# Kernel tuning notes

Measured on AMD Instinct MI355X. Metric: run time of the kernel, lower is better.

Reference implementation:

```python
import jax, jax.numpy as jnp
import numpy as np

H, D, L = 4, 64, 7          # heads, hidden, seq_len (SEQ_LEN+2)
B = 32768                    # batch
VOCAB = 6
NOUT = 2 * 5 + 1             # 2*SEQ_LEN+1 = 11
EPS = 1e-5


def _ln(x, g, b):
    m = jnp.mean(x, axis=-1, keepdims=True)
    v = jnp.var(x, axis=-1, keepdims=True)
    return (x - m) / jnp.sqrt(v + EPS) * g + b


def _mha(q, k, v, wq, wk, wv, wo, bo):
    # wq/wk/wv: [H, D, D]; q: [B, Lq, D]; k,v: [B, Lk, D]
    qh = jnp.einsum('bqd,hde->hbqe', q, wq)
    kh = jnp.einsum('bkd,hde->hbke', k, wk)
    vh = jnp.einsum('bkd,hde->hbke', v, wv)
    s = jnp.einsum('hbqe,hbke->hbqk', qh, kh) / jnp.sqrt(jnp.asarray(D, q.dtype))
    # NOTE: original torch code softmaxes over dim=1 of [B,Lq,Lk] = the QUERY axis
    a = jax.nn.softmax(s, axis=2)
    o = jnp.einsum('hbqk,hbke->hbqe', a, vh)
    o = jnp.transpose(o, (1, 2, 0, 3)).reshape(q.shape[0], q.shape[1], H * D)
    return o @ wo + bo


def setup_inputs() -> dict:
    key = jax.random.key(0)
    ks = iter(jax.random.split(key, 32))
    n = lambda shape, s=0.02: jax.random.normal(next(ks), shape, dtype=jnp.float32) * s
    inp = {
        'tokens': jax.random.randint(next(ks), (B, L), 0, VOCAB, dtype=jnp.int32),
        'emb': n((VOCAB, D), 1.0),
        'pos': n((L, 1), 1.0),
        'qparam': n((1, D), 1.0),
        'in_w': n((D + 1, D)), 'in_b': n((D,)),
        # encoding layer (num_encoding_layers=1)
        'e_wq': n((H, D, D)), 'e_wk': n((H, D, D)), 'e_wv': n((H, D, D)),
        'e_wo': n((H * D, D)), 'e_bo': n((D,)),
        'e_g1': jnp.ones((D,), jnp.float32), 'e_b1': jnp.zeros((D,), jnp.float32),
        'e_c1w': n((D, 2 * D)), 'e_c1b': n((2 * D,)),
        'e_c2w': n((2 * D, D)), 'e_c2b': n((D,)),
        'e_g2': jnp.ones((D,), jnp.float32), 'e_b2': jnp.zeros((D,), jnp.float32),
        # decoder MHA
        'd_wq': n((H, D, D)), 'd_wk': n((H, D, D)), 'd_wv': n((H, D, D)),
        'd_wo': n((H * D, D)), 'd_bo': n((D,)),
        'fc_w': n((D, NOUT)), 'fc_b': n((NOUT,)),
    }
    return inp


def reference(tokens, emb, pos, qparam, in_w, in_b,
              e_wq, e_wk, e_wv, e_wo, e_bo, e_g1, e_b1,
              e_c1w, e_c1b, e_c2w, e_c2b, e_g2, e_b2,
              d_wq, d_wk, d_wv, d_wo, d_bo, fc_w, fc_b):
    x = emb[tokens]                                   # [B, L, D]
    p = jnp.broadcast_to(pos[None], (x.shape[0], L, 1))
    x = jnp.concatenate([x, p], axis=-1)              # [B, L, D+1]
    x = x @ in_w + in_b                               # Conv1d k=1 == linear
    # encoding layer
    x = _mha(x, x, x, e_wq, e_wk, e_wv, e_wo, e_bo)
    x = _ln(x, e_g1, e_b1)
    x1 = jax.nn.relu(x @ e_c1w + e_c1b)
    x1 = jax.nn.relu(x1 @ e_c2w + e_c2b)
    x = _ln(x + x1, e_g2, e_b2)
    # decoder: single learned query
    q = jnp.broadcast_to(qparam[None], (x.shape[0], 1, D))
    x = _mha(q, x, x, d_wq, d_wk, d_wv, d_wo, d_bo)   # [B, 1, D]
    x = x[:, 0, :]
    return x @ fc_w + fc_b                            # [B, 11]
```

## Files before the change

### kernel.cpp

```cpp
#include <hip/hip_runtime.h>
#include <hip/hip_bf16.h>

#define DEV __device__ __forceinline__

typedef __attribute__((ext_vector_type(8)))  short bf8v;
typedef __attribute__((ext_vector_type(16))) float f16v;
typedef __attribute__((ext_vector_type(4)))  float f4v;

static constexpr int NOUT = 11;

DEV unsigned short b16(float f){
  __hip_bfloat16 h = __float2bfloat16(f);
  unsigned short s; __builtin_memcpy(&s, &h, 2); return s;
}
DEV float bf2f(unsigned short s){
  __hip_bfloat16 h; __builtin_memcpy(&h, &s, 2); return __bfloat162float(h);
}
template<bool BF16>
DEV float ldw(const void* p, int i){
  if constexpr (BF16) return bf2f(((const unsigned short*)p)[i]);
  else return ((const float*)p)[i];
}
DEV f16v MF(bf8v a, bf8v b, f16v c){
  return __builtin_amdgcn_mfma_f32_32x32x16_bf16(a, b, c, 0, 0, 0);
}
DEV f16v zf(){ f16v v; 
  #pragma unroll
  for (int i=0;i<16;++i) v[i] = 0.f; 
  return v; }


__global__ void k_flag(const void* g1, unsigned* flag){
  if (threadIdx.x == 0){
    unsigned bits = *(const unsigned*)g1;
    *flag = (bits == 0x3F800000u) ? 0u : 1u;
  }
}

struct RawW {
  const void *in_w, *in_b, *pos;
  const void *e_wq, *e_wk, *e_wv, *e_wo, *e_bo;
  const void *g1, *b1, *c1w, *c1b, *c2w, *c2b, *g2, *b2;
};
struct PackP {
  unsigned short *Wt, *Mt, *Ut, *C1t, *C2t;
  float *BB;
};

template<bool BF16>
DEV void prepack_impl(int blk, int t, const RawW r, PackP p){
  if (blk < 256){
    int g = blk*64 + t; int h = g >> 12; int rr = g & 4095; int n = rr >> 6; int k = rr & 63;
    float acc = 0.f;
    for (int e = 0; e < 64; ++e)
      acc += ldw<BF16>(r.e_wq, h*4096 + k*64 + e) * ldw<BF16>(r.e_wk, h*4096 + n*64 + e);
    p.Mt[g] = b16(acc * 0.125f);
  } else if (blk < 512){
    int g = (blk-256)*64 + t; int h = g >> 12; int rr = g & 4095; int n = rr >> 6; int k = rr & 63;
    float acc = 0.f;
    for (int e = 0; e < 64; ++e)
      acc += ldw<BF16>(r.e_wv, h*4096 + k*64 + e) * ldw<BF16>(r.e_wo, (h*64+e)*64 + n);
    p.Ut[g] = b16(acc);
  } else if (blk < 528){
    for (int i = 0; i < 8; ++i){
      int idx = (blk-512)*512 + i*64 + t;
      int n = idx >> 6, k = idx & 63;
      p.C1t[idx] = b16(ldw<BF16>(r.c1w, k*128 + n));
    }
  } else if (blk < 544){
    for (int i = 0; i < 8; ++i){
      int idx = (blk-528)*512 + i*64 + t;
      int n = idx >> 7, k = idx & 127;
      p.C2t[idx] = b16(ldw<BF16>(r.c2w, k*64 + n));
    }
  } else if (blk < 552){
    for (int i = 0; i < 8; ++i){
      int idx = (blk-544)*512 + i*64 + t;
      int n = idx >> 6, k = idx & 63;
      p.Wt[idx] = b16(ldw<BF16>(r.in_w, k*64 + n));
    }
  } else if (blk == 552){
    for (int i = 0; i < 8; ++i){
      int idx = i*64 + t; int l = idx >> 6, n = idx & 63;
      float v = 0.f;
      if (l < 7) v = ldw<BF16>(r.in_b, n) + ldw<BF16>(r.pos, l) * ldw<BF16>(r.in_w, 64*64 + n);
      p.BB[idx] = v;
    }
  } else {
    for (int i = 0; i < 8; ++i){
      int idx = i*64 + t;
      float v;
      if      (idx < 64 ) v = ldw<BF16>(r.e_bo, idx);
      else if (idx < 192) v = ldw<BF16>(r.c1b, idx-64);
      else if (idx < 256) v = ldw<BF16>(r.c2b, idx-192);
      else if (idx < 320) v = ldw<BF16>(r.g1,  idx-256);
      else if (idx < 384) v = ldw<BF16>(r.b1,  idx-320);
      else if (idx < 448) v = ldw<BF16>(r.g2,  idx-384);
      else                v = ldw<BF16>(r.b2,  idx-448);
      p.BB[512 + idx] = v;
    }
  }
}
__global__ void k_prepack(const unsigned* flag, RawW r, PackP p){
  if (*flag) prepack_impl<true >(blockIdx.x, threadIdx.x, r, p);
  else       prepack_impl<false>(blockIdx.x, threadIdx.x, r, p);
}

template<bool BF16>
DEV float wdec_acc(const void* wv, const void* wo, int d, int ep){
  float acc = 0.f;
  for (int h = 0; h < 4; ++h)
    for (int e = 0; e < 64; ++e)
      acc += ldw<BF16>(wv, (h*64+d)*64 + e) * ldw<BF16>(wo, (h*64+e)*64 + ep);
  return acc;
}
__global__ void k_wdec(const unsigned* flag, const void* wv, const void* wo, float* Wdec){
  int t = blockIdx.x*64 + threadIdx.x;
  int d = t >> 6, ep = t & 63;
  Wdec[t] = (*flag) ? wdec_acc<true>(wv,wo,d,ep) : wdec_acc<false>(wv,wo,d,ep);
}
template<bool BF16>
DEV void wfin_impl(int t, const float* Wdec, const void* fc_w, const void* fc_b,
                   const void* d_bo, float* WfT, float* bfin){
  if (t < 704){
    int j = t >> 6, d = t & 63;
    float acc = 0.f;
    for (int ep = 0; ep < 64; ++ep) acc += Wdec[d*64+ep] * ldw<BF16>(fc_w, ep*11 + j);
    WfT[j*64 + d] = acc;
  } else if (t < 715){
    int j = t - 704;
    float acc = ldw<BF16>(fc_b, j);
    for (int ep = 0; ep < 64; ++ep) acc += ldw<BF16>(d_bo, ep) * ldw<BF16>(fc_w, ep*11 + j);
    bfin[j] = acc;
  }
}
__global__ void k_wfinal(const unsigned* flag, const float* Wdec, const void* fc_w,
                         const void* fc_b, const void* d_bo, float* WfT, float* bfin){
  if (*flag) wfin_impl<true >(threadIdx.x, Wdec, fc_w, fc_b, d_bo, WfT, bfin);
  else       wfin_impl<false>(threadIdx.x, Wdec, fc_w, fc_b, d_bo, WfT, bfin);
}

struct KP {
  const int* tokens;
  const void* emb;
  const unsigned* flagp;
  const unsigned short *Wt, *Mt, *Ut, *C1t, *C2t;
  const float *BB, *WfT, *bfin;
  void* out;
};

DEV void gemm_ct(const unsigned short* Wg, const short* Xl, int l31, int koff,
                 f16v& a0, f16v& a1){
  #pragma unroll
  for (int s = 0; s < 4; ++s){
    bf8v xb = *(const bf8v*)(Xl + l31*72 + koff + 16*s);
    bf8v w0 = *(const bf8v*)(Wg + l31*64 + koff + 16*s);
    bf8v w1 = *(const bf8v*)(Wg + (32+l31)*64 + koff + 16*s);
    a0 = MF(w0, xb, a0);
    a1 = MF(w1, xb, a1);
  }
}
DEV void store_ct(short* dst, int l31, int sub, const f16v& a, int ft){
  #pragma unroll
  for (int run = 0; run < 4; ++run){
    int f0 = ft*32 + sub*4 + run*8;
    ushort4 u;
    u.x = b16(a[run*4+0]); u.y = b16(a[run*4+1]);
    u.z = b16(a[run*4+2]); u.w = b16(a[run*4+3]);
    *(ushort4*)(dst + l31*72 + f0) = u;
  }
}

__global__ __launch_bounds__(256, 3) void k_main(KP kp){
  __shared__ __align__(16) char smem[53248];
  const int tid  = threadIdx.x;
  const int lane = tid & 63;
  const int wave = tid >> 6;
  const int l31  = lane & 31;
  const int sub  = lane >> 5;
  const int koff = sub * 8;
  const unsigned flagv = *kp.flagp;

  float* Bpos  = (float*)(smem + 49152);
  float* biasf = Bpos + 512;
  for (int i = tid; i < 1024; i += 256) Bpos[i] = kp.BB[i];
  __syncthreads();

  short* Xw  = (short*)(smem + wave*12288);
  short* scr = (short*)(smem + wave*12288 + 4608);
  short* Tt  = scr;
  short* Zt  = scr;
  short* Pr  = scr + 2560;
  short* H1  = scr;
  float* xsb = (float*)scr;

  const int grp   = blockIdx.x*4 + wave;
  const int item0 = grp*4;

  {
    int c = lane & 7, pos = lane >> 3;
    #pragma unroll 1
    for (int it = 0; it < 4; ++it){
      int row = it*8 + pos;
      short* dst = Xw + row*72 + c*8;
      if (pos < 7){
        int tok = kp.tokens[(item0+it)*7 + pos];
        if (flagv){
          *(uint4*)dst = *(const uint4*)((const unsigned short*)kp.emb + tok*64 + c*8);
        } else {
          const float* e = (const float*)kp.emb + tok*64 + c*8;
          ushort4 u0, u1;
          u0.x=b16(e[0]); u0.y=b16(e[1]); u0.z=b16(e[2]); u0.w=b16(e[3]);
          u1.x=b16(e[4]); u1.y=b16(e[5]); u1.z=b16(e[6]); u1.w=b16(e[7]);
          *(ushort4*)dst = u0; *(ushort4*)(dst+4) = u1;
        }
      } else {
        uint4 z; z.x=z.y=z.z=z.w=0u;
        *(uint4*)dst = z;
      }
    }
  }

  {
    f16v a0 = zf(), a1 = zf();
    gemm_ct(kp.Wt, Xw, l31, koff, a0, a1);
    const float* bp = Bpos + (l31 & 7)*64;
    #pragma unroll
    for (int run = 0; run < 4; ++run){
      f4v v0 = *(const f4v*)(bp + sub*4 + run*8);
      f4v v1 = *(const f4v*)(bp + 32 + sub*4 + run*8);
      #pragma unroll
      for (int q = 0; q < 4; ++q){ a0[run*4+q] += v0[q]; a1[run*4+q] += v1[q]; }
    }
    store_ct(Xw, l31, sub, a0, 0);
    store_ct(Xw, l31, sub, a1, 1);
  }

  f16v o0, o1;
  {
    const float* bo = biasf;
    #pragma unroll
    for (int run = 0; run < 4; ++run){
      f4v v0 = *(const f4v*)(bo + sub*4 + run*8);
      f4v v1 = *(const f4v*)(bo + 32 + sub*4 + run*8);
      #pragma unroll
      for (int q = 0; q < 4; ++q){ o0[run*4+q] = v0[q]; o1[run*4+q] = v1[q]; }
    }
  }
  const int jm = l31 >> 3;
  #pragma unroll 1
  for (int h = 0; h < 4; ++h){
    const unsigned short* Mh = kp.Mt + h*4096;
    const unsigned short* Uh = kp.Ut + h*4096;
    {
      f16v t0 = zf(), t1 = zf();
      gemm_ct(Mh, Xw, l31, koff, t0, t1);
      store_ct(Tt, l31, sub, t0, 0);
      store_ct(Tt, l31, sub, t1, 1);
    }
    f16v sc = zf();
    #pragma unroll
    for (int s = 0; s < 4; ++s){
      bf8v ta = *(const bf8v*)(Tt + l31*72 + koff + 16*s);
      bf8v xb = *(const bf8v*)(Xw + l31*72 + koff + 16*s);
      sc = MF(ta, xb, sc);
    }
    float s0=0.f, s1=0.f, s2=0.f, s3=0.f;
    #pragma unroll
    for (int r4 = 0; r4 < 4; ++r4){
      if (r4 == jm){ s0 = sc[r4*4+0]; s1 = sc[r4*4+1]; s2 = sc[r4*4+2]; s3 = sc[r4*4+3]; }
    }
    float s3m = sub ? -3.0e38f : s3;
    float mx = fmaxf(fmaxf(s0, s1), fmaxf(s2, s3m));
    mx = fmaxf(mx, __shfl_xor(mx, 32));
    float e0 = __expf(s0-mx), e1 = __expf(s1-mx), e2 = __expf(s2-mx);
    float e3 = sub ? 0.f : __expf(s3-mx);
    float sum = e0+e1+e2+e3;
    sum += __shfl_xor(sum, 32);
    float inv = 1.f / sum;
    float p0 = e0*inv, p1 = e1*inv, p2 = e2*inv, p3 = e3*inv;
    #pragma unroll
    for (int r = 0; r < 16; ++r){
      int q = (r&3) + 8*(r>>2) + 4*sub;
      float v = 0.f;
      if ((r>>2) == jm) v = (r&3)==0 ? p0 : (r&3)==1 ? p1 : (r&3)==2 ? p2 : p3;
      Pr[q*40 + l31] = b16(v);
    }
    {
      f16v z0 = zf(), z1 = zf();
      #pragma unroll
      for (int s = 0; s < 4; ++s){
        bf8v xa = *(const bf8v*)(Xw + l31*72 + koff + 16*s);
        bf8v u0 = *(const bf8v*)(Uh + l31*64 + koff + 16*s);
        bf8v u1 = *(const bf8v*)(Uh + (32+l31)*64 + koff + 16*s);
        z0 = MF(xa, u0, z0);
        z1 = MF(xa, u1, z1);
      }
      #pragma unroll
      for (int nt = 0; nt < 2; ++nt){
        const f16v& z = nt ? z1 : z0;
        #pragma unroll
        for (int run = 0; run < 4; ++run){
          int r0 = sub*4 + run*8;
          ushort4 u;
          u.x = b16(z[run*4+0]); u.y = b16(z[run*4+1]);
          u.z = b16(z[run*4+2]); u.w = b16(z[run*4+3]);
          *(ushort4*)(Zt + (nt*32 + l31)*40 + r0) = u;
        }
      }
    }
    #pragma unroll
    for (int s = 0; s < 2; ++s){
      bf8v pb  = *(const bf8v*)(Pr + l31*40 + koff + 16*s);
      bf8v za0 = *(const bf8v*)(Zt + l31*40 + koff + 16*s);
      bf8v za1 = *(const bf8v*)(Zt + (32+l31)*40 + koff + 16*s);
      o0 = MF(za0, pb, o0);
      o1 = MF(za1, pb, o1);
    }
  }

  {
    float sm = 0.f, sq = 0.f;
    #pragma unroll
    for (int r = 0; r < 16; ++r){ sm += o0[r] + o1[r]; sq += o0[r]*o0[r] + o1[r]*o1[r]; }
    sm += __shfl_xor(sm, 32);
    sq += __shfl_xor(sq, 32);
    float mean = sm * 0.015625f;
    float var  = sq * 0.015625f - mean*mean;
    float rs = rsqrtf(var + 1e-5f);
    const float* g1 = biasf + 256;
    const float* b1 = biasf + 320;
    #pragma unroll
    for (int run = 0; run < 4; ++run){
      f4v ga = *(const f4v*)(g1 + sub*4 + run*8);
      f4v ba = *(const f4v*)(b1 + sub*4 + run*8);
      f4v gb = *(const f4v*)(g1 + 32 + sub*4 + run*8);
      f4v bb = *(const f4v*)(b1 + 32 + sub*4 + run*8);
      ushort4 u0, u1;
      u0.x = b16((o0[run*4+0]-mean)*rs*ga[0] + ba[0]);
      u0.y = b16((o0[run*4+1]-mean)*rs*ga[1] + ba[1]);
      u0.z = b16((o0[run*4+2]-mean)*rs*ga[2] + ba[2]);
      u0.w = b16((o0[run*4+3]-mean)*rs*ga[3] + ba[3]);
      u1.x = b16((o1[run*4+0]-mean)*rs*gb[0] + bb[0]);
      u1.y = b16((o1[run*4+1]-mean)*rs*gb[1] + bb[1]);
      u1.z = b16((o1[run*4+2]-mean)*rs*gb[2] + bb[2]);
      u1.w = b16((o1[run*4+3]-mean)*rs*gb[3] + bb[3]);
      *(ushort4*)(Xw + l31*72 + sub*4 + run*8) = u0;
      *(ushort4*)(Xw + l31*72 + 32 + sub*4 + run*8) = u1;
    }
  }

  f16v f2a = zf(), f2b = zf();
  #pragma unroll 1
  for (int hf = 0; hf < 2; ++hf){
    f16v h0 = zf(), h1 = zf();
    gemm_ct(kp.C1t + hf*4096, Xw, l31, koff, h0, h1);
    const float* c1b = biasf + 64 + hf*64;
    #pragma unroll
    for (int run = 0; run < 4; ++run){
      f4v v0 = *(const f4v*)(c1b + sub*4 + run*8);
      f4v v1 = *(const f4v*)(c1b + 32 + sub*4 + run*8);
      #pragma unroll
      for (int q = 0; q < 4; ++q){
        h0[run*4+q] = fmaxf(h0[run*4+q] + v0[q], 0.f);
        h1[run*4+q] = fmaxf(h1[run*4+q] + v1[q], 0.f);
      }
    }
    store_ct(H1, l31, sub, h0, 0);
    store_ct(H1, l31, sub, h1, 1);
    #pragma unroll
    for (int s = 0; s < 4; ++s){
      bf8v hb = *(const bf8v*)(H1 + l31*72 + koff + 16*s);
      bf8v w0 = *(const bf8v*)(kp.C2t + l31*128 + hf*64 + koff + 16*s);
      bf8v w1 = *(const bf8v*)(kp.C2t + (32+l31)*128 + hf*64 + koff + 16*s);
      f2a = MF(w0, hb, f2a);
      f2b = MF(w1, hb, f2b);
    }
  }

  float xf0[16], xf1[16];
  {
    const float* c2b = biasf + 192;
    #pragma unroll
    for (int run = 0; run < 4; ++run){
      f4v v0 = *(const f4v*)(c2b + sub*4 + run*8);
      f4v v1 = *(const f4v*)(c2b + 32 + sub*4 + run*8);
      ushort4 r0 = *(const ushort4*)(Xw + l31*72 + sub*4 + run*8);
      ushort4 r1 = *(const ushort4*)(Xw + l31*72 + 32 + sub*4 + run*8);
      xf0[run*4+0] = bf2f(r0.x) + fmaxf(f2a[run*4+0] + v0[0], 0.f);
      xf0[run*4+1] = bf2f(r0.y) + fmaxf(f2a[run*4+1] + v0[1], 0.f);
      xf0[run*4+2] = bf2f(r0.z) + fmaxf(f2a[run*4+2] + v0[2], 0.f);
      xf0[run*4+3] = bf2f(r0.w) + fmaxf(f2a[run*4+3] + v0[3], 0.f);
      xf1[run*4+0] = bf2f(r1.x) + fmaxf(f2b[run*4+0] + v1[0], 0.f);
      xf1[run*4+1] = bf2f(r1.y) + fmaxf(f2b[run*4+1] + v1[1], 0.f);
      xf1[run*4+2] = bf2f(r1.z) + fmaxf(f2b[run*4+2] + v1[2], 0.f);
      xf1[run*4+3] = bf2f(r1.w) + fmaxf(f2b[run*4+3] + v1[3], 0.f);
    }
    float sm = 0.f, sq = 0.f;
    #pragma unroll
    for (int r = 0; r < 16; ++r){ sm += xf0[r] + xf1[r]; sq += xf0[r]*xf0[r] + xf1[r]*xf1[r]; }
    sm += __shfl_xor(sm, 32);
    sq += __shfl_xor(sq, 32);
    float mean = sm * 0.015625f;
    float var  = sq * 0.015625f - mean*mean;
    float rs = rsqrtf(var + 1e-5f);
    const float* g2 = biasf + 384;
    const float* b2 = biasf + 448;
    #pragma unroll
    for (int run = 0; run < 4; ++run){
      f4v ga = *(const f4v*)(g2 + sub*4 + run*8);
      f4v ba = *(const f4v*)(b2 + sub*4 + run*8);
      f4v gb = *(const f4v*)(g2 + 32 + sub*4 + run*8);
      f4v bb = *(const f4v*)(b2 + 32 + sub*4 + run*8);
      #pragma unroll
      for (int q = 0; q < 4; ++q){
        xf0[run*4+q] = (xf0[run*4+q] - mean)*rs*ga[q] + ba[q];
        xf1[run*4+q] = (xf1[run*4+q] - mean)*rs*gb[q] + bb[q];
      }
    }
  }

  if ((l31 & 7) == 7){
    #pragma unroll
    for (int r = 0; r < 16; ++r){ xf0[r] = 0.f; xf1[r] = 0.f; }
  }
  #pragma unroll
  for (int r = 0; r < 16; ++r){
    float v0 = xf0[r], v1 = xf1[r];
    v0 += __shfl_xor(v0, 1); v0 += __shfl_xor(v0, 2); v0 += __shfl_xor(v0, 4);
    v1 += __shfl_xor(v1, 1); v1 += __shfl_xor(v1, 2); v1 += __shfl_xor(v1, 4);
    xf0[r] = v0; xf1[r] = v1;
  }
  if ((l31 & 7) == 0){
    int it = l31 >> 3;
    #pragma unroll
    for (int run = 0; run < 4; ++run){
      f4v v0, v1;
      #pragma unroll
      for (int q = 0; q < 4; ++q){ v0[q] = xf0[run*4+q]; v1[q] = xf1[run*4+q]; }
      *(f4v*)(xsb + it*64 + sub*4 + run*8) = v0;
      *(f4v*)(xsb + it*64 + 32 + sub*4 + run*8) = v1;
    }
  }
  if (lane < 44){
    int it = lane / 11, j = lane - it*11;
    float acc = kp.bfin[j];
    const float* xr = xsb + it*64;
    const float* wr = kp.WfT + j*64;
    #pragma unroll
    for (int k4 = 0; k4 < 64; k4 += 4){
      f4v xv = *(const f4v*)(xr + k4);
      f4v wv = *(const f4v*)(wr + k4);
      acc += xv[0]*wv[0] + xv[1]*wv[1] + xv[2]*wv[2] + xv[3]*wv[3];
    }
    int gi = item0 + it;
    if (flagv) ((__hip_bfloat16*)kp.out)[gi*NOUT + j] = __float2bfloat16(acc);
    else       ((float*)kp.out)[gi*NOUT + j] = acc;
  }
}

extern "C" void kernel_launch(void* const* d_in, const int* in_sizes, int n_in,
                              void* d_out, int out_size, void* d_ws, size_t ws_size,
                              hipStream_t stream){
  const int* tokens = (const int*)d_in[0];
  const void* emb = d_in[1];
  RawW r { d_in[4], d_in[5], d_in[2],
           d_in[6], d_in[7], d_in[8], d_in[9], d_in[10],
           d_in[11], d_in[12], d_in[13], d_in[14], d_in[15], d_in[16], d_in[17], d_in[18] };

  char* ws = (char*)d_ws;
  unsigned* flag = (unsigned*)(ws + 0);
  float* BB   = (float*)(ws + 16);
  float* WfT  = (float*)(ws + 4112);
  float* bfin = (float*)(ws + 6928);
  float* Wdec = (float*)(ws + 6976);
  unsigned short* Wt  = (unsigned short*)(ws + 23360);
  unsigned short* Mt  = (unsigned short*)(ws + 31552);
  unsigned short* Ut  = (unsigned short*)(ws + 64320);
  unsigned short* C1t = (unsigned short*)(ws + 97088);
  unsigned short* C2t = (unsigned short*)(ws + 113472);

  k_flag<<<1, 64, 0, stream>>>(d_in[11], flag);
  PackP p { Wt, Mt, Ut, C1t, C2t, BB };
  k_prepack<<<554, 64, 0, stream>>>(flag, r, p);
  k_wdec<<<64, 64, 0, stream>>>(flag, d_in[21], d_in[22], Wdec);
  k_wfinal<<<1, 768, 0, stream>>>(flag, Wdec, d_in[24], d_in[25], d_in[23], WfT, bfin);

  KP kp { tokens, emb, flag, Wt, Mt, Ut, C1t, C2t, BB, WfT, bfin, d_out };
  k_main<<<2048, 256, 0, stream>>>(kp);
}
```

Baseline: 242.1 us.

## Keep MFMA operands in registers via lane shuffles and merge prep kernels

The main kernel now passes intermediate GEMM results straight into the next MFMA operand layout. It packs accumulators to bf16 pairs and swaps halves across lanes with shfl_xor, where before it stored them to padded LDS and read them back. Per-wave LDS drops from 12 KB to 4 KB with an XOR-swizzled layout, and launch bounds rise to 4 blocks per CU for higher occupancy. The setup side drops the separate flag kernel and merges prepack plus the decoder-weight fold into two kernels with larger blocks, cutting launch overhead. The cost is extra shuffle and pack instructions and more register pressure under the tighter occupancy bound.

```diff
diff --git a/kernel.cpp b/kernel.cpp
--- a/kernel.cpp
+++ b/kernel.cpp
@@ -15,6 +15,9 @@
 }
 DEV float bf2f(unsigned short s){
   __hip_bfloat16 h; __builtin_memcpy(&h, &s, 2); return __bfloat162float(h);
+}
+DEV unsigned pk2(float lo, float hi){
+  return (unsigned)b16(lo) | ((unsigned)b16(hi) << 16);
 }
 template<bool BF16>
 DEV float ldw(const void* p, int i){
@@ -24,18 +27,41 @@
 DEV f16v MF(bf8v a, bf8v b, f16v c){
   return __builtin_amdgcn_mfma_f32_32x32x16_bf16(a, b, c, 0, 0, 0);
 }
-DEV f16v zf(){ f16v v; 
+DEV f16v zf(){ f16v v;
   #pragma unroll
-  for (int i=0;i<16;++i) v[i] = 0.f; 
+  for (int i=0;i<16;++i) v[i]=0.f;
   return v; }
-
-
-__global__ void k_flag(const void* g1, unsigned* flag){
-  if (threadIdx.x == 0){
-    unsigned bits = *(const unsigned*)g1;
-    *flag = (bits == 0x3F800000u) ? 0u : 1u;
-  }
-}
+DEV bf8v g16(const unsigned short* p){ return *(const bf8v*)p; }
+
+struct PkTile { unsigned u[8]; };
+DEV PkTile pack_tile(const f16v& a){
+  PkTile t;
+  #pragma unroll
+  for (int j=0;j<8;++j) t.u[j] = pk2(a[2*j], a[2*j+1]);
+  return t;
+}
+DEV bf8v as8(unsigned a, unsigned b, unsigned c, unsigned d){
+  union { unsigned u[4]; bf8v v; } x;
+  x.u[0]=a; x.u[1]=b; x.u[2]=c; x.u[3]=d; return x.v;
+}
+DEV void exch(const PkTile& t, int sub, bf8v& k0, bf8v& k1){
+  unsigned sa = sub ? t.u[0] : t.u[2];
+  unsigned sb = sub ? t.u[1] : t.u[3];
+  unsigned sc = sub ? t.u[4] : t.u[6];
+  unsigned sd = sub ? t.u[5] : t.u[7];
+  unsigned ra = __shfl_xor(sa, 32);
+  unsigned rb = __shfl_xor(sb, 32);
+  unsigned rc = __shfl_xor(sc, 32);
+  unsigned rd = __shfl_xor(sd, 32);
+  if (sub == 0){
+    k0 = as8(t.u[0], t.u[1], ra, rb);
+    k1 = as8(t.u[4], t.u[5], rc, rd);
+  } else {
+    k0 = as8(ra, rb, t.u[2], t.u[3]);
+    k1 = as8(rc, rd, t.u[6], t.u[7]);
+  }
+}
+
 
 struct RawW {
   const void *in_w, *in_b, *pos;
@@ -48,171 +74,145 @@
 };
 
 template<bool BF16>
-DEV void prepack_impl(int blk, int t, const RawW r, PackP p){
-  if (blk < 256){
-    int g = blk*64 + t; int h = g >> 12; int rr = g & 4095; int n = rr >> 6; int k = rr & 63;
+DEV void prep_impl(int b, int t, const RawW r, PackP p){
+  if (b < 64){
+    int idx = b*256 + t;
+    int h = idx >> 12, rr = idx & 4095, n = rr >> 6, k = rr & 63;
     float acc = 0.f;
-    for (int e = 0; e < 64; ++e)
+    #pragma unroll 8
+    for (int e=0;e<64;++e)
       acc += ldw<BF16>(r.e_wq, h*4096 + k*64 + e) * ldw<BF16>(r.e_wk, h*4096 + n*64 + e);
-    p.Mt[g] = b16(acc * 0.125f);
-  } else if (blk < 512){
-    int g = (blk-256)*64 + t; int h = g >> 12; int rr = g & 4095; int n = rr >> 6; int k = rr & 63;
+    p.Mt[idx] = b16(acc * 0.125f);
+  } else if (b < 128){
+    int idx = (b-64)*256 + t;
+    int h = idx >> 12, rr = idx & 4095, n = rr >> 6, k = rr & 63;
     float acc = 0.f;
-    for (int e = 0; e < 64; ++e)
+    #pragma unroll 8
+    for (int e=0;e<64;++e)
       acc += ldw<BF16>(r.e_wv, h*4096 + k*64 + e) * ldw<BF16>(r.e_wo, (h*64+e)*64 + n);
-    p.Ut[g] = b16(acc);
-  } else if (blk < 528){
-    for (int i = 0; i < 8; ++i){
-      int idx = (blk-512)*512 + i*64 + t;
-      int n = idx >> 6, k = idx & 63;
+    p.Ut[idx] = b16(acc);
+  } else if (b == 128){
+    for (int i=0;i<32;++i){
+      int idx = i*256 + t; int n = idx >> 6, k = idx & 63;
       p.C1t[idx] = b16(ldw<BF16>(r.c1w, k*128 + n));
     }
-  } else if (blk < 544){
-    for (int i = 0; i < 8; ++i){
-      int idx = (blk-528)*512 + i*64 + t;
-      int n = idx >> 7, k = idx & 127;
+  } else if (b == 129){
+    for (int i=0;i<32;++i){
+      int idx = i*256 + t; int n = idx >> 7, k = idx & 127;
       p.C2t[idx] = b16(ldw<BF16>(r.c2w, k*64 + n));
     }
-  } else if (blk < 552){
-    for (int i = 0; i < 8; ++i){
-      int idx = (blk-544)*512 + i*64 + t;
-      int n = idx >> 6, k = idx & 63;
+  } else if (b == 130){
+    for (int i=0;i<16;++i){
+      int idx = i*256 + t; int n = idx >> 6, k = idx & 63;
       p.Wt[idx] = b16(ldw<BF16>(r.in_w, k*64 + n));
     }
-  } else if (blk == 552){
-    for (int i = 0; i < 8; ++i){
-      int idx = i*64 + t; int l = idx >> 6, n = idx & 63;
-      float v = 0.f;
-      if (l < 7) v = ldw<BF16>(r.in_b, n) + ldw<BF16>(r.pos, l) * ldw<BF16>(r.in_w, 64*64 + n);
+  } else {
+    for (int i=0;i<4;++i){
+      int idx = i*256 + t;
+      float v;
+      if (idx < 512){
+        int l = idx >> 6, n = idx & 63;
+        v = (l < 7) ? ldw<BF16>(r.in_b, n) + ldw<BF16>(r.pos, l) * ldw<BF16>(r.in_w, 64*64 + n)
+                    : 0.f;
+      } else {
+        int q = idx - 512;
+        if      (q < 64 ) v = ldw<BF16>(r.e_bo, q);
+        else if (q < 192) v = ldw<BF16>(r.c1b, q-64);
+        else if (q < 256) v = ldw<BF16>(r.c2b, q-192);
+        else if (q < 320) v = ldw<BF16>(r.g1,  q-256);
+        else if (q < 384) v = ldw<BF16>(r.b1,  q-320);
+        else if (q < 448) v = ldw<BF16>(r.g2,  q-384);
+        else              v = ldw<BF16>(r.b2,  q-448);
+      }
       p.BB[idx] = v;
     }
-  } else {
-    for (int i = 0; i < 8; ++i){
-      int idx = i*64 + t;
-      float v;
-      if      (idx < 64 ) v = ldw<BF16>(r.e_bo, idx);
-      else if (idx < 192) v = ldw<BF16>(r.c1b, idx-64);
-      else if (idx < 256) v = ldw<BF16>(r.c2b, idx-192);
-      else if (idx < 320) v = ldw<BF16>(r.g1,  idx-256);
-      else if (idx < 384) v = ldw<BF16>(r.b1,  idx-320);
-      else if (idx < 448) v = ldw<BF16>(r.g2,  idx-384);
-      else                v = ldw<BF16>(r.b2,  idx-448);
-      p.BB[512 + idx] = v;
-    }
-  }
-}
-__global__ void k_prepack(const unsigned* flag, RawW r, PackP p){
-  if (*flag) prepack_impl<true >(blockIdx.x, threadIdx.x, r, p);
-  else       prepack_impl<false>(blockIdx.x, threadIdx.x, r, p);
+  }
+}
+__global__ void k_prep(RawW r, PackP p){
+  bool bf = (*(const unsigned*)r.g1) != 0x3F800000u;
+  if (bf) prep_impl<true >(blockIdx.x, threadIdx.x, r, p);
+  else    prep_impl<false>(blockIdx.x, threadIdx.x, r, p);
 }
 
 template<bool BF16>
-DEV float wdec_acc(const void* wv, const void* wo, int d, int ep){
-  float acc = 0.f;
-  for (int h = 0; h < 4; ++h)
-    for (int e = 0; e < 64; ++e)
-      acc += ldw<BF16>(wv, (h*64+d)*64 + e) * ldw<BF16>(wo, (h*64+e)*64 + ep);
-  return acc;
-}
-__global__ void k_wdec(const unsigned* flag, const void* wv, const void* wo, float* Wdec){
-  int t = blockIdx.x*64 + threadIdx.x;
-  int d = t >> 6, ep = t & 63;
-  Wdec[t] = (*flag) ? wdec_acc<true>(wv,wo,d,ep) : wdec_acc<false>(wv,wo,d,ep);
-}
-template<bool BF16>
-DEV void wfin_impl(int t, const float* Wdec, const void* fc_w, const void* fc_b,
-                   const void* d_bo, float* WfT, float* bfin){
+DEV void dec_impl(int t, const void* d_wv, const void* d_wo, const void* fc_w,
+                  const void* fc_b, const void* d_bo, float* G, float* WfT, float* bfin){
+  for (int g = t; g < 2816; g += 1024){
+    int he = g / 11, j = g - he*11;
+    float acc = 0.f;
+    #pragma unroll 8
+    for (int ep=0; ep<64; ++ep)
+      acc += ldw<BF16>(d_wo, he*64+ep) * ldw<BF16>(fc_w, ep*11+j);
+    G[g] = acc;
+  }
+  __syncthreads();
   if (t < 704){
     int j = t >> 6, d = t & 63;
     float acc = 0.f;
-    for (int ep = 0; ep < 64; ++ep) acc += Wdec[d*64+ep] * ldw<BF16>(fc_w, ep*11 + j);
+    #pragma unroll 8
+    for (int he=0; he<256; ++he)
+      acc += ldw<BF16>(d_wv, (he>>6)*4096 + d*64 + (he&63)) * G[he*11 + j];
     WfT[j*64 + d] = acc;
   } else if (t < 715){
     int j = t - 704;
     float acc = ldw<BF16>(fc_b, j);
-    for (int ep = 0; ep < 64; ++ep) acc += ldw<BF16>(d_bo, ep) * ldw<BF16>(fc_w, ep*11 + j);
+    #pragma unroll 8
+    for (int ep=0; ep<64; ++ep)
+      acc += ldw<BF16>(d_bo, ep) * ldw<BF16>(fc_w, ep*11+j);
     bfin[j] = acc;
   }
 }
-__global__ void k_wfinal(const unsigned* flag, const float* Wdec, const void* fc_w,
-                         const void* fc_b, const void* d_bo, float* WfT, float* bfin){
-  if (*flag) wfin_impl<true >(threadIdx.x, Wdec, fc_w, fc_b, d_bo, WfT, bfin);
-  else       wfin_impl<false>(threadIdx.x, Wdec, fc_w, fc_b, d_bo, WfT, bfin);
+__global__ void k_dec(const void* g1, const void* d_wv, const void* d_wo, const void* fc_w,
+                      const void* fc_b, const void* d_bo, float* WfT, float* bfin){
+  __shared__ float G[2816];
+  bool bf = (*(const unsigned*)g1) != 0x3F800000u;
+  if (bf) dec_impl<true >(threadIdx.x, d_wv, d_wo, fc_w, fc_b, d_bo, G, WfT, bfin);
+  else    dec_impl<false>(threadIdx.x, d_wv, d_wo, fc_w, fc_b, d_bo, G, WfT, bfin);
 }
 
 struct KP {
   const int* tokens;
   const void* emb;
-  const unsigned* flagp;
+  const void* g1;
   const unsigned short *Wt, *Mt, *Ut, *C1t, *C2t;
   const float *BB, *WfT, *bfin;
   void* out;
 };
 
-DEV void gemm_ct(const unsigned short* Wg, const short* Xl, int l31, int koff,
-                 f16v& a0, f16v& a1){
-  #pragma unroll
-  for (int s = 0; s < 4; ++s){
-    bf8v xb = *(const bf8v*)(Xl + l31*72 + koff + 16*s);
-    bf8v w0 = *(const bf8v*)(Wg + l31*64 + koff + 16*s);
-    bf8v w1 = *(const bf8v*)(Wg + (32+l31)*64 + koff + 16*s);
-    a0 = MF(w0, xb, a0);
-    a1 = MF(w1, xb, a1);
-  }
-}
-DEV void store_ct(short* dst, int l31, int sub, const f16v& a, int ft){
-  #pragma unroll
-  for (int run = 0; run < 4; ++run){
-    int f0 = ft*32 + sub*4 + run*8;
-    ushort4 u;
-    u.x = b16(a[run*4+0]); u.y = b16(a[run*4+1]);
-    u.z = b16(a[run*4+2]); u.w = b16(a[run*4+3]);
-    *(ushort4*)(dst + l31*72 + f0) = u;
-  }
-}
-
-__global__ __launch_bounds__(256, 3) void k_main(KP kp){
-  __shared__ __align__(16) char smem[53248];
+__global__ __launch_bounds__(256, 4) void k_main(KP kp){
+  __shared__ __align__(16) char smem[4*4096 + 4096];
   const int tid  = threadIdx.x;
   const int lane = tid & 63;
   const int wave = tid >> 6;
   const int l31  = lane & 31;
   const int sub  = lane >> 5;
-  const int koff = sub * 8;
-  const unsigned flagv = *kp.flagp;
-
-  float* Bpos  = (float*)(smem + 49152);
+  const int jm   = l31 >> 3;
+  const bool isbf = (*(const unsigned*)kp.g1) != 0x3F800000u;
+
+  float* Bpos  = (float*)(smem + 16384);
   float* biasf = Bpos + 512;
+  #pragma unroll
   for (int i = tid; i < 1024; i += 256) Bpos[i] = kp.BB[i];
-  __syncthreads();
-
-  short* Xw  = (short*)(smem + wave*12288);
-  short* scr = (short*)(smem + wave*12288 + 4608);
-  short* Tt  = scr;
-  short* Zt  = scr;
-  short* Pr  = scr + 2560;
-  short* H1  = scr;
-  float* xsb = (float*)scr;
-
-  const int grp   = blockIdx.x*4 + wave;
-  const int item0 = grp*4;
+
+  short* Xw = (short*)(smem + wave*4096);
+  const int item0 = (blockIdx.x*4 + wave)*4;
 
   {
     int c = lane & 7, pos = lane >> 3;
     #pragma unroll 1
-    for (int it = 0; it < 4; ++it){
+    for (int it=0; it<4; ++it){
       int row = it*8 + pos;
-      short* dst = Xw + row*72 + c*8;
+      short* dst = Xw + row*64 + ((c ^ pos)*8);
       if (pos < 7){
         int tok = kp.tokens[(item0+it)*7 + pos];
-        if (flagv){
+        if (isbf){
           *(uint4*)dst = *(const uint4*)((const unsigned short*)kp.emb + tok*64 + c*8);
         } else {
           const float* e = (const float*)kp.emb + tok*64 + c*8;
-          ushort4 u0, u1;
-          u0.x=b16(e[0]); u0.y=b16(e[1]); u0.z=b16(e[2]); u0.w=b16(e[3]);
-          u1.x=b16(e[4]); u1.y=b16(e[5]); u1.z=b16(e[6]); u1.w=b16(e[7]);
-          *(ushort4*)dst = u0; *(ushort4*)(dst+4) = u1;
+          uint4 u;
+          u.x = pk2(e[0], e[1]); u.y = pk2(e[2], e[3]);
+          u.z = pk2(e[4], e[5]); u.w = pk2(e[6], e[7]);
+          *(uint4*)dst = u;
         }
       } else {
         uint4 z; z.x=z.y=z.z=z.w=0u;
@@ -220,161 +220,172 @@
       }
     }
   }
-
+  __syncthreads();
+
+  bf8v xk[4];
   {
     f16v a0 = zf(), a1 = zf();
-    gemm_ct(kp.Wt, Xw, l31, koff, a0, a1);
+    #pragma unroll
+    for (int s=0;s<4;++s){
+      bf8v xb = *(const bf8v*)(Xw + l31*64 + (((2*s+sub) ^ (l31&7))*8));
+      bf8v w0 = g16(kp.Wt + l31*64 + s*16 + sub*8);
+      bf8v w1 = g16(kp.Wt + (32+l31)*64 + s*16 + sub*8);
+      a0 = MF(w0, xb, a0);
+      a1 = MF(w1, xb, a1);
+    }
     const float* bp = Bpos + (l31 & 7)*64;
     #pragma unroll
-    for (int run = 0; run < 4; ++run){
+    for (int run=0; run<4; ++run){
       f4v v0 = *(const f4v*)(bp + sub*4 + run*8);
       f4v v1 = *(const f4v*)(bp + 32 + sub*4 + run*8);
       #pragma unroll
-      for (int q = 0; q < 4; ++q){ a0[run*4+q] += v0[q]; a1[run*4+q] += v1[q]; }
-    }
-    store_ct(Xw, l31, sub, a0, 0);
-    store_ct(Xw, l31, sub, a1, 1);
+      for (int q=0;q<4;++q){ a0[run*4+q] += v0[q]; a1[run*4+q] += v1[q]; }
+    }
+    PkTile px0 = pack_tile(a0), px1 = pack_tile(a1);
+    exch(px0, sub, xk[0], xk[1]);
+    exch(px1, sub, xk[2], xk[3]);
+  }
+
+  short* Pr = Xw;
+  {
+    uint4 z; z.x=z.y=z.z=z.w=0u;
+    *(uint4*)(Pr + lane*16)     = z;
+    *(uint4*)(Pr + lane*16 + 8) = z;
   }
 
   f16v o0, o1;
   {
     const float* bo = biasf;
     #pragma unroll
-    for (int run = 0; run < 4; ++run){
+    for (int run=0; run<4; ++run){
       f4v v0 = *(const f4v*)(bo + sub*4 + run*8);
       f4v v1 = *(const f4v*)(bo + 32 + sub*4 + run*8);
       #pragma unroll
-      for (int q = 0; q < 4; ++q){ o0[run*4+q] = v0[q]; o1[run*4+q] = v1[q]; }
-    }
-  }
-  const int jm = l31 >> 3;
+      for (int q=0;q<4;++q){ o0[run*4+q] = v0[q]; o1[run*4+q] = v1[q]; }
+    }
+  }
   #pragma unroll 1
-  for (int h = 0; h < 4; ++h){
+  for (int h=0; h<4; ++h){
     const unsigned short* Mh = kp.Mt + h*4096;
     const unsigned short* Uh = kp.Ut + h*4096;
-    {
-      f16v t0 = zf(), t1 = zf();
-      gemm_ct(Mh, Xw, l31, koff, t0, t1);
-      store_ct(Tt, l31, sub, t0, 0);
-      store_ct(Tt, l31, sub, t1, 1);
-    }
+    f16v t0 = zf(), t1 = zf();
+    #pragma unroll
+    for (int s=0;s<4;++s){
+      bf8v m0 = g16(Mh + l31*64 + s*16 + sub*8);
+      bf8v m1 = g16(Mh + (32+l31)*64 + s*16 + sub*8);
+      t0 = MF(m0, xk[s], t0);
+      t1 = MF(m1, xk[s], t1);
+    }
+    PkTile pt0 = pack_tile(t0), pt1 = pack_tile(t1);
+    bf8v tA[4];
+    exch(pt0, sub, tA[0], tA[1]);
+    exch(pt1, sub, tA[2], tA[3]);
     f16v sc = zf();
     #pragma unroll
-    for (int s = 0; s < 4; ++s){
-      bf8v ta = *(const bf8v*)(Tt + l31*72 + koff + 16*s);
-      bf8v xb = *(const bf8v*)(Xw + l31*72 + koff + 16*s);
-      sc = MF(ta, xb, sc);
-    }
+    for (int s=0;s<4;++s) sc = MF(tA[s], xk[s], sc);
+
     float s0=0.f, s1=0.f, s2=0.f, s3=0.f;
     #pragma unroll
-    for (int r4 = 0; r4 < 4; ++r4){
-      if (r4 == jm){ s0 = sc[r4*4+0]; s1 = sc[r4*4+1]; s2 = sc[r4*4+2]; s3 = sc[r4*4+3]; }
+    for (int r4=0;r4<4;++r4){
+      if (r4 == jm){ s0=sc[r4*4+0]; s1=sc[r4*4+1]; s2=sc[r4*4+2]; s3=sc[r4*4+3]; }
     }
     float s3m = sub ? -3.0e38f : s3;
-    float mx = fmaxf(fmaxf(s0, s1), fmaxf(s2, s3m));
+    float mx = fmaxf(fmaxf(s0,s1), fmaxf(s2,s3m));
     mx = fmaxf(mx, __shfl_xor(mx, 32));
-    float e0 = __expf(s0-mx), e1 = __expf(s1-mx), e2 = __expf(s2-mx);
+    float e0=__expf(s0-mx), e1=__expf(s1-mx), e2=__expf(s2-mx);
     float e3 = sub ? 0.f : __expf(s3-mx);
     float sum = e0+e1+e2+e3;
     sum += __shfl_xor(sum, 32);
-    float inv = 1.f / sum;
-    float p0 = e0*inv, p1 = e1*inv, p2 = e2*inv, p3 = e3*inv;
-    #pragma unroll
-    for (int r = 0; r < 16; ++r){
-      int q = (r&3) + 8*(r>>2) + 4*sub;
-      float v = 0.f;
-      if ((r>>2) == jm) v = (r&3)==0 ? p0 : (r&3)==1 ? p1 : (r&3)==2 ? p2 : p3;
-      Pr[q*40 + l31] = b16(v);
-    }
-    {
-      f16v z0 = zf(), z1 = zf();
-      #pragma unroll
-      for (int s = 0; s < 4; ++s){
-        bf8v xa = *(const bf8v*)(Xw + l31*72 + koff + 16*s);
-        bf8v u0 = *(const bf8v*)(Uh + l31*64 + koff + 16*s);
-        bf8v u1 = *(const bf8v*)(Uh + (32+l31)*64 + koff + 16*s);
-        z0 = MF(xa, u0, z0);
-        z1 = MF(xa, u1, z1);
-      }
-      #pragma unroll
-      for (int nt = 0; nt < 2; ++nt){
-        const f16v& z = nt ? z1 : z0;
-        #pragma unroll
-        for (int run = 0; run < 4; ++run){
-          int r0 = sub*4 + run*8;
-          ushort4 u;
-          u.x = b16(z[run*4+0]); u.y = b16(z[run*4+1]);
-          u.z = b16(z[run*4+2]); u.w = b16(z[run*4+3]);
-          *(ushort4*)(Zt + (nt*32 + l31)*40 + r0) = u;
-        }
-      }
-    }
-    #pragma unroll
-    for (int s = 0; s < 2; ++s){
-      bf8v pb  = *(const bf8v*)(Pr + l31*40 + koff + 16*s);
-      bf8v za0 = *(const bf8v*)(Zt + l31*40 + koff + 16*s);
-      bf8v za1 = *(const bf8v*)(Zt + (32+l31)*40 + koff + 16*s);
-      o0 = MF(za0, pb, o0);
-      o1 = MF(za1, pb, o1);
-    }
-  }
-
+    float inv = 1.f/sum;
+    float pv[4] = {e0*inv, e1*inv, e2*inv, e3*inv};
+    #pragma unroll
+    for (int i=0;i<4;++i){
+      int q = jm*8 + 4*sub + i;
+      Pr[q*32 + ((jm ^ i)*8) + (l31 & 7)] = (short)b16(pv[i]);
+    }
+
+    f16v z0 = zf(), z1 = zf();
+    #pragma unroll
+    for (int s=0;s<4;++s){
+      bf8v u0 = g16(Uh + l31*64 + s*16 + sub*8);
+      bf8v u1 = g16(Uh + (32+l31)*64 + s*16 + sub*8);
+      z0 = MF(xk[s], u0, z0);
+      z1 = MF(xk[s], u1, z1);
+    }
+    PkTile pz0 = pack_tile(z0), pz1 = pack_tile(z1);
+    bf8v zA[4];
+    exch(pz0, sub, zA[0], zA[1]);
+    exch(pz1, sub, zA[2], zA[3]);
+    bf8v pb0 = *(const bf8v*)(Pr + l31*32 + (((sub  ) ^ (l31&3))*8));
+    bf8v pb1 = *(const bf8v*)(Pr + l31*32 + (((2+sub) ^ (l31&3))*8));
+    o0 = MF(zA[0], pb0, o0);
+    o0 = MF(zA[1], pb1, o0);
+    o1 = MF(zA[2], pb0, o1);
+    o1 = MF(zA[3], pb1, o1);
+  }
+
+  f16v xl0, xl1;
   {
-    float sm = 0.f, sq = 0.f;
-    #pragma unroll
-    for (int r = 0; r < 16; ++r){ sm += o0[r] + o1[r]; sq += o0[r]*o0[r] + o1[r]*o1[r]; }
+    float sm=0.f, sq=0.f;
+    #pragma unroll
+    for (int r=0;r<16;++r){ sm += o0[r]+o1[r]; sq += o0[r]*o0[r] + o1[r]*o1[r]; }
     sm += __shfl_xor(sm, 32);
     sq += __shfl_xor(sq, 32);
     float mean = sm * 0.015625f;
     float var  = sq * 0.015625f - mean*mean;
     float rs = rsqrtf(var + 1e-5f);
-    const float* g1 = biasf + 256;
-    const float* b1 = biasf + 320;
-    #pragma unroll
-    for (int run = 0; run < 4; ++run){
-      f4v ga = *(const f4v*)(g1 + sub*4 + run*8);
-      f4v ba = *(const f4v*)(b1 + sub*4 + run*8);
-      f4v gb = *(const f4v*)(g1 + 32 + sub*4 + run*8);
-      f4v bb = *(const f4v*)(b1 + 32 + sub*4 + run*8);
-      ushort4 u0, u1;
-      u0.x = b16((o0[run*4+0]-mean)*rs*ga[0] + ba[0]);
-      u0.y = b16((o0[run*4+1]-mean)*rs*ga[1] + ba[1]);
-      u0.z = b16((o0[run*4+2]-mean)*rs*ga[2] + ba[2]);
-      u0.w = b16((o0[run*4+3]-mean)*rs*ga[3] + ba[3]);
-      u1.x = b16((o1[run*4+0]-mean)*rs*gb[0] + bb[0]);
-      u1.y = b16((o1[run*4+1]-mean)*rs*gb[1] + bb[1]);
-      u1.z = b16((o1[run*4+2]-mean)*rs*gb[2] + bb[2]);
-      u1.w = b16((o1[run*4+3]-mean)*rs*gb[3] + bb[3]);
-      *(ushort4*)(Xw + l31*72 + sub*4 + run*8) = u0;
-      *(ushort4*)(Xw + l31*72 + 32 + sub*4 + run*8) = u1;
-    }
-  }
+    const float* g1v = biasf + 256;
+    const float* b1v = biasf + 320;
+    #pragma unroll
+    for (int run=0; run<4; ++run){
+      f4v ga = *(const f4v*)(g1v + sub*4 + run*8);
+      f4v ba = *(const f4v*)(b1v + sub*4 + run*8);
+      f4v gb = *(const f4v*)(g1v + 32 + sub*4 + run*8);
+      f4v bb = *(const f4v*)(b1v + 32 + sub*4 + run*8);
+      #pragma unroll
+      for (int q=0;q<4;++q){
+        xl0[run*4+q] = (o0[run*4+q]-mean)*rs*ga[q] + ba[q];
+        xl1[run*4+q] = (o1[run*4+q]-mean)*rs*gb[q] + bb[q];
+      }
+    }
+  }
+  PkTile pxl0 = pack_tile(xl0), pxl1 = pack_tile(xl1);
+  bf8v hxk[4];
+  exch(pxl0, sub, hxk[0], hxk[1]);
+  exch(pxl1, sub, hxk[2], hxk[3]);
 
   f16v f2a = zf(), f2b = zf();
   #pragma unroll 1
-  for (int hf = 0; hf < 2; ++hf){
+  for (int hf=0; hf<2; ++hf){
     f16v h0 = zf(), h1 = zf();
-    gemm_ct(kp.C1t + hf*4096, Xw, l31, koff, h0, h1);
+    #pragma unroll
+    for (int s=0;s<4;++s){
+      bf8v c0 = g16(kp.C1t + (hf*64 + l31)*64 + s*16 + sub*8);
+      bf8v c1 = g16(kp.C1t + (hf*64 + 32 + l31)*64 + s*16 + sub*8);
+      h0 = MF(c0, hxk[s], h0);
+      h1 = MF(c1, hxk[s], h1);
+    }
     const float* c1b = biasf + 64 + hf*64;
     #pragma unroll
-    for (int run = 0; run < 4; ++run){
+    for (int run=0; run<4; ++run){
       f4v v0 = *(const f4v*)(c1b + sub*4 + run*8);
       f4v v1 = *(const f4v*)(c1b + 32 + sub*4 + run*8);
       #pragma unroll
-      for (int q = 0; q < 4; ++q){
-        h0[run*4+q] = fmaxf(h0[run*4+q] + v0[q], 0.f);
-        h1[run*4+q] = fmaxf(h1[run*4+q] + v1[q], 0.f);
+      for (int q=0;q<4;++q){
+        h0[run*4+q] = fmaxf(h0[run*4+q]+v0[q], 0.f);
+        h1[run*4+q] = fmaxf(h1[run*4+q]+v1[q], 0.f);
       }
     }
-    store_ct(H1, l31, sub, h0, 0);
-    store_ct(H1, l31, sub, h1, 1);
-    #pragma unroll
-    for (int s = 0; s < 4; ++s){
-      bf8v hb = *(const bf8v*)(H1 + l31*72 + koff + 16*s);
-      bf8v w0 = *(const bf8v*)(kp.C2t + l31*128 + hf*64 + koff + 16*s);
-      bf8v w1 = *(const bf8v*)(kp.C2t + (32+l31)*128 + hf*64 + koff + 16*s);
-      f2a = MF(w0, hb, f2a);
-      f2b = MF(w1, hb, f2b);
+    PkTile q0 = pack_tile(h0), q1 = pack_tile(h1);
+    bf8v hk[4];
+    exch(q0, sub, hk[0], hk[1]);
+    exch(q1, sub, hk[2], hk[3]);
+    #pragma unroll
+    for (int s=0;s<4;++s){
+      bf8v w0 = g16(kp.C2t + l31*128 + hf*64 + s*16 + sub*8);
+      bf8v w1 = g16(kp.C2t + (32+l31)*128 + hf*64 + s*16 + sub*8);
+      f2a = MF(w0, hk[s], f2a);
+      f2b = MF(w1, hk[s], f2b);
     }
   }
 
@@ -382,62 +393,63 @@
   {
     const float* c2b = biasf + 192;
     #pragma unroll
-    for (int run = 0; run < 4; ++run){
+    for (int run=0; run<4; ++run){
       f4v v0 = *(const f4v*)(c2b + sub*4 + run*8);
       f4v v1 = *(const f4v*)(c2b + 32 + sub*4 + run*8);
-      ushort4 r0 = *(const ushort4*)(Xw + l31*72 + sub*4 + run*8);
-      ushort4 r1 = *(const ushort4*)(Xw + l31*72 + 32 + sub*4 + run*8);
-      xf0[run*4+0] = bf2f(r0.x) + fmaxf(f2a[run*4+0] + v0[0], 0.f);
-      xf0[run*4+1] = bf2f(r0.y) + fmaxf(f2a[run*4+1] + v0[1], 0.f);
-      xf0[run*4+2] = bf2f(r0.z) + fmaxf(f2a[run*4+2] + v0[2], 0.f);
-      xf0[run*4+3] = bf2f(r0.w) + fmaxf(f2a[run*4+3] + v0[3], 0.f);
-      xf1[run*4+0] = bf2f(r1.x) + fmaxf(f2b[run*4+0] + v1[0], 0.f);
-      xf1[run*4+1] = bf2f(r1.y) + fmaxf(f2b[run*4+1] + v1[1], 0.f);
-      xf1[run*4+2] = bf2f(r1.z) + fmaxf(f2b[run*4+2] + v1[2], 0.f);
-      xf1[run*4+3] = bf2f(r1.w) + fmaxf(f2b[run*4+3] + v1[3], 0.f);
-    }
-    float sm = 0.f, sq = 0.f;
-    #pragma unroll
-    for (int r = 0; r < 16; ++r){ sm += xf0[r] + xf1[r]; sq += xf0[r]*xf0[r] + xf1[r]*xf1[r]; }
+      #pragma unroll
+      for (int q=0;q<4;++q){
+        int r = run*4+q;
+        float res0 = (r&1) ? bf2f((unsigned short)(pxl0.u[r>>1] >> 16))
+                           : bf2f((unsigned short)(pxl0.u[r>>1] & 0xffffu));
+        float res1 = (r&1) ? bf2f((unsigned short)(pxl1.u[r>>1] >> 16))
+                           : bf2f((unsigned short)(pxl1.u[r>>1] & 0xffffu));
+        xf0[r] = res0 + fmaxf(f2a[r] + v0[q], 0.f);
+        xf1[r] = res1 + fmaxf(f2b[r] + v1[q], 0.f);
+      }
+    }
+    float sm=0.f, sq=0.f;
+    #pragma unroll
+    for (int r=0;r<16;++r){ sm += xf0[r]+xf1[r]; sq += xf0[r]*xf0[r] + xf1[r]*xf1[r]; }
     sm += __shfl_xor(sm, 32);
     sq += __shfl_xor(sq, 32);
     float mean = sm * 0.015625f;
     float var  = sq * 0.015625f - mean*mean;
     float rs = rsqrtf(var + 1e-5f);
-    const float* g2 = biasf + 384;
-    const float* b2 = biasf + 448;
-    #pragma unroll
-    for (int run = 0; run < 4; ++run){
-      f4v ga = *(const f4v*)(g2 + sub*4 + run*8);
-      f4v ba = *(const f4v*)(b2 + sub*4 + run*8);
-      f4v gb = *(const f4v*)(g2 + 32 + sub*4 + run*8);
-      f4v bb = *(const f4v*)(b2 + 32 + sub*4 + run*8);
-      #pragma unroll
-      for (int q = 0; q < 4; ++q){
-        xf0[run*4+q] = (xf0[run*4+q] - mean)*rs*ga[q] + ba[q];
-        xf1[run*4+q] = (xf1[run*4+q] - mean)*rs*gb[q] + bb[q];
+    const float* g2v = biasf + 384;
+    const float* b2v = biasf + 448;
+    #pragma unroll
+    for (int run=0; run<4; ++run){
+      f4v ga = *(const f4v*)(g2v + sub*4 + run*8);
+      f4v ba = *(const f4v*)(b2v + sub*4 + run*8);
+      f4v gb = *(const f4v*)(g2v + 32 + sub*4 + run*8);
+      f4v bb = *(const f4v*)(b2v + 32 + sub*4 + run*8);
+      #pragma unroll
+      for (int q=0;q<4;++q){
+        xf0[run*4+q] = (xf0[run*4+q]-mean)*rs*ga[q] + ba[q];
+        xf1[run*4+q] = (xf1[run*4+q]-mean)*rs*gb[q] + bb[q];
       }
     }
   }
 
   if ((l31 & 7) == 7){
     #pragma unroll
-    for (int r = 0; r < 16; ++r){ xf0[r] = 0.f; xf1[r] = 0.f; }
+    for (int r=0;r<16;++r){ xf0[r]=0.f; xf1[r]=0.f; }
   }
   #pragma unroll
-  for (int r = 0; r < 16; ++r){
+  for (int r=0;r<16;++r){
     float v0 = xf0[r], v1 = xf1[r];
-    v0 += __shfl_xor(v0, 1); v0 += __shfl_xor(v0, 2); v0 += __shfl_xor(v0, 4);
-    v1 += __shfl_xor(v1, 1); v1 += __shfl_xor(v1, 2); v1 += __shfl_xor(v1, 4);
-    xf0[r] = v0; xf1[r] = v1;
-  }
+    v0 += __shfl_xor(v0,1); v0 += __shfl_xor(v0,2); v0 += __shfl_xor(v0,4);
+    v1 += __shfl_xor(v1,1); v1 += __shfl_xor(v1,2); v1 += __shfl_xor(v1,4);
+    xf0[r]=v0; xf1[r]=v1;
+  }
+  float* xsb = (float*)Pr;
   if ((l31 & 7) == 0){
     int it = l31 >> 3;
     #pragma unroll
-    for (int run = 0; run < 4; ++run){
+    for (int run=0; run<4; ++run){
       f4v v0, v1;
       #pragma unroll
-      for (int q = 0; q < 4; ++q){ v0[q] = xf0[run*4+q]; v1[q] = xf1[run*4+q]; }
+      for (int q=0;q<4;++q){ v0[q]=xf0[run*4+q]; v1[q]=xf1[run*4+q]; }
       *(f4v*)(xsb + it*64 + sub*4 + run*8) = v0;
       *(f4v*)(xsb + it*64 + 32 + sub*4 + run*8) = v1;
     }
@@ -448,14 +460,14 @@
     const float* xr = xsb + it*64;
     const float* wr = kp.WfT + j*64;
     #pragma unroll
-    for (int k4 = 0; k4 < 64; k4 += 4){
+    for (int k4=0;k4<64;k4+=4){
       f4v xv = *(const f4v*)(xr + k4);
       f4v wv = *(const f4v*)(wr + k4);
-      acc += xv[0]*wv[0] + xv[1]*wv[1] + xv[2]*wv[2] + xv[3]*wv[3];
+      acc += xv[0]*wv[0]+xv[1]*wv[1]+xv[2]*wv[2]+xv[3]*wv[3];
     }
     int gi = item0 + it;
-    if (flagv) ((__hip_bfloat16*)kp.out)[gi*NOUT + j] = __float2bfloat16(acc);
-    else       ((float*)kp.out)[gi*NOUT + j] = acc;
+    if (isbf) ((__hip_bfloat16*)kp.out)[gi*NOUT+j] = __float2bfloat16(acc);
+    else      ((float*)kp.out)[gi*NOUT+j] = acc;
   }
 }
 
@@ -464,28 +476,26 @@
                               hipStream_t stream){
   const int* tokens = (const int*)d_in[0];
   const void* emb = d_in[1];
+  const void* g1  = d_in[11];
   RawW r { d_in[4], d_in[5], d_in[2],
            d_in[6], d_in[7], d_in[8], d_in[9], d_in[10],
            d_in[11], d_in[12], d_in[13], d_in[14], d_in[15], d_in[16], d_in[17], d_in[18] };
 
   char* ws = (char*)d_ws;
-  unsigned* flag = (unsigned*)(ws + 0);
-  float* BB   = (float*)(ws + 16);
-  float* WfT  = (float*)(ws + 4112);
-  float* bfin = (float*)(ws + 6928);
-  float* Wdec = (float*)(ws + 6976);
-  unsigned short* Wt  = (unsigned short*)(ws + 23360);
-  unsigned short* Mt  = (unsigned short*)(ws + 31552);
-  unsigned short* Ut  = (unsigned short*)(ws + 64320);
-  unsigned short* C1t = (unsigned short*)(ws + 97088);
-  unsigned short* C2t = (unsigned short*)(ws + 113472);
-
-  k_flag<<<1, 64, 0, stream>>>(d_in[11], flag);
+  float* BB   = (float*)(ws + 0);
+  float* WfT  = (float*)(ws + 4096);
+  float* bfin = (float*)(ws + 6912);
+  unsigned short* Wt  = (unsigned short*)(ws + 8192);
+  unsigned short* Mt  = (unsigned short*)(ws + 16384);
+  unsigned short* Ut  = (unsigned short*)(ws + 49152);
+  unsigned short* C1t = (unsigned short*)(ws + 81920);
+  unsigned short* C2t = (unsigned short*)(ws + 98304);
+
   PackP p { Wt, Mt, Ut, C1t, C2t, BB };
-  k_prepack<<<554, 64, 0, stream>>>(flag, r, p);
-  k_wdec<<<64, 64, 0, stream>>>(flag, d_in[21], d_in[22], Wdec);
-  k_wfinal<<<1, 768, 0, stream>>>(flag, Wdec, d_in[24], d_in[25], d_in[23], WfT, bfin);
-
-  KP kp { tokens, emb, flag, Wt, Mt, Ut, C1t, C2t, BB, WfT, bfin, d_out };
+  k_prep<<<132, 256, 0, stream>>>(r, p);
+  k_dec<<<1, 1024, 0, stream>>>(g1, d_in[21], d_in[22], d_in[24], d_in[25], d_in[23],
+                                WfT, bfin);
+
+  KP kp { tokens, emb, g1, Wt, Mt, Ut, C1t, C2t, BB, WfT, bfin, d_out };
   k_main<<<2048, 256, 0, stream>>>(kp);
 }
```

Result: slower. 327.8 us (+35.4%).
